# Performance work log

Hardware: AMD Instinct MI355X
Metric: run time of the kernel (lower is better)

Reference implementation:

```python
import jax, jax.numpy as jnp
import numpy as np

B, S, D = 2, 2048, 4096
H, KVH = 32, 8
DH = D // H  # 128
N_REP = H // KVH
ROPE_BASE = 10000.0


def _rope_tables(seq_len, d_head, dtype):
    inv_freq = 1.0 / (ROPE_BASE ** (jnp.arange(0, d_head, 2, dtype=jnp.float32) / d_head))
    pos = jnp.arange(seq_len, dtype=jnp.float32)
    freqs = pos[:, None] * inv_freq[None, :]            # (S, DH/2)
    emb = jnp.concatenate([freqs, freqs], axis=-1)       # (S, DH)
    return jnp.cos(emb).astype(dtype), jnp.sin(emb).astype(dtype)


def _rotate_half(x):
    half = x.shape[-1] // 2
    return jnp.concatenate([-x[..., half:], x[..., :half]], axis=-1)


def _apply_rope(x, cos, sin):
    # x: (B, h, S, DH); cos/sin: (S, DH)
    return x * cos[None, None, :, :] + _rotate_half(x) * sin[None, None, :, :]


def setup_inputs() -> dict:
    key = jax.random.key(0)
    ks = jax.random.split(key, 6)
    scale = 0.02
    return {
        "x": jax.random.normal(ks[0], (B, S, D), dtype=jnp.float32),
        "Wq": jax.random.normal(ks[1], (D, H * DH), dtype=jnp.float32) * scale,
        "Wk": jax.random.normal(ks[2], (D, KVH * DH), dtype=jnp.float32) * scale,
        "Wv": jax.random.normal(ks[3], (D, KVH * DH), dtype=jnp.float32) * scale,
        "Wo": jax.random.normal(ks[4], (D, D), dtype=jnp.float32) * scale,
        "bo": jnp.zeros((D,), dtype=jnp.float32),
    }


def reference(x, Wq, Wk, Wv, Wo, bo):
    b, s, _ = x.shape
    # QKV projections (no bias)
    q = (x @ Wq).reshape(b, s, H, DH).transpose(0, 2, 1, 3)    # (B, H, S, DH)
    k = (x @ Wk).reshape(b, s, KVH, DH).transpose(0, 2, 1, 3)  # (B, KVH, S, DH)
    v = (x @ Wv).reshape(b, s, KVH, DH).transpose(0, 2, 1, 3)
    # RoPE on q and k
    cos, sin = _rope_tables(s, DH, x.dtype)
    q = _apply_rope(q, cos, sin)
    k = _apply_rope(k, cos, sin)
    # GQA: repeat KV heads to match query heads
    k = jnp.repeat(k, N_REP, axis=1)  # (B, H, S, DH)
    v = jnp.repeat(v, N_REP, axis=1)
    # Causal scaled dot-product attention
    scale = 1.0 / jnp.sqrt(jnp.asarray(DH, dtype=x.dtype))
    scores = jnp.einsum("bhqd,bhkd->bhqk", q, k) * scale       # (B, H, S, S)
    causal = jnp.tril(jnp.ones((s, s), dtype=bool))
    scores = jnp.where(causal[None, None, :, :], scores, jnp.finfo(x.dtype).min)
    attn = jax.nn.softmax(scores, axis=-1)
    out = jnp.einsum("bhqk,bhkd->bhqd", attn, v)               # (B, H, S, DH)
    out = out.transpose(0, 2, 1, 3).reshape(b, s, H * DH)
    return out @ Wo + bo
```

## Files before the change

kernel.cpp:

```cpp
#include <hip/hip_runtime.h>

typedef unsigned short u16;
typedef unsigned int u32;
typedef __attribute__((ext_vector_type(8))) short s16x8;
typedef __attribute__((ext_vector_type(8))) u16 u16x8;
typedef __attribute__((ext_vector_type(4))) float f32x4;
typedef __attribute__((ext_vector_type(4))) u32 u32x4;

#define SEQ 2048
#define NH 32
#define NKV 8

__device__ __forceinline__ u16 f2bf(float f) {
  union { float f; u32 u; } v; v.f = f;
  u32 r = v.u + 0x7FFFu + ((v.u >> 16) & 1u);
  return (u16)(r >> 16);
}
__device__ __forceinline__ float bf2f(u16 u) {
  union { u32 u; float f; } v; v.u = ((u32)u) << 16;
  return v.f;
}
__device__ __forceinline__ u32 pack2(float a, float b) {
  return (u32)f2bf(a) | ((u32)f2bf(b) << 16);
}
__device__ __forceinline__ void gll16(u16* lds, const u16* g) {
  __builtin_amdgcn_global_load_lds(
      (const __attribute__((address_space(1))) u32*)g,
      (__attribute__((address_space(3))) u32*)lds, 16, 0, 0);
}

__global__ void k_conv_bf16(const float* __restrict__ in, u16* __restrict__ out) {
  long i = ((long)blockIdx.x * 256 + threadIdx.x) * 4;
  const float4 v = *(const float4*)&in[i];
  ushort4 ov = { f2bf(v.x), f2bf(v.y), f2bf(v.z), f2bf(v.w) };
  *(ushort4*)&out[i] = ov;
}

__global__ void k_transpose_bf16(const float* __restrict__ W, u16* __restrict__ Wt,
                                 int K, int N) {
  __shared__ u16 T[64 * 65];
  int n0 = blockIdx.x * 64, k0 = blockIdx.y * 64;
  int t = threadIdx.x;
  int cr = t >> 4, cc = (t & 15) * 4;
#pragma unroll
  for (int r2 = 0; r2 < 4; ++r2) {
    int k = cr + r2 * 16;
    const float4 v = *(const float4*)&W[(long)(k0 + k) * N + n0 + cc];
    u16* d = &T[k * 65 + cc];
    d[0] = f2bf(v.x); d[1] = f2bf(v.y); d[2] = f2bf(v.z); d[3] = f2bf(v.w);
  }
  __syncthreads();
#pragma unroll
  for (int r2 = 0; r2 < 4; ++r2) {
    int n = cr + r2 * 16;
    ushort4 ov = { T[(cc + 0) * 65 + n], T[(cc + 1) * 65 + n],
                   T[(cc + 2) * 65 + n], T[(cc + 3) * 65 + n] };
    *(ushort4*)&Wt[(long)(n0 + n) * K + k0 + cc] = ov;
  }
}

__global__ void k_vt(const u16* __restrict__ Vb, u16* __restrict__ Vt) {
  __shared__ u16 T[64][136];
  int s0 = blockIdx.x * 64;
  int g = blockIdx.y;
  const u16* src = Vb + (long)g * SEQ * 128;
  u16* dst = Vt + (long)g * 128 * SEQ;
  int t = threadIdx.x;
#pragma unroll
  for (int i = 0; i < 4; ++i) {
    int c = i * 256 + t;
    int row = c >> 4, col8 = (c & 15) * 8;
    u16x8 v = *(const u16x8*)&src[(long)(s0 + row) * 128 + col8];
#pragma unroll
    for (int j = 0; j < 8; ++j) T[row][col8 + j] = v[j];
  }
  __syncthreads();
#pragma unroll
  for (int i = 0; i < 4; ++i) {
    int c = i * 256 + t;
    int d = c >> 3, k8 = (c & 7) * 8;
    u16x8 v;
#pragma unroll
    for (int j = 0; j < 8; ++j) v[j] = T[k8 + j][d];
    *(u16x8*)&dst[(long)d * SEQ + s0 + k8] = v;
  }
}

__global__ void k_rope_table(float* __restrict__ cosT, float* __restrict__ sinT) {
  int id = blockIdx.x * 256 + threadIdx.x;
  int s = id >> 6, i = id & 63;
  float inv = powf(10000.0f, -(float)i * (1.0f / 64.0f));
  float f = (float)s * inv;
  float sv, cv;
  sincosf(f, &sv, &cv);
  cosT[id] = cv; sinT[id] = sv;
}

__global__ void k_rope_apply(u16* __restrict__ Qb, u16* __restrict__ Kb,
                             const float* __restrict__ cosT, const float* __restrict__ sinT) {
  int id = blockIdx.x * 256 + threadIdx.x;
  int i = id & 63;
  int row = id >> 6;
  u16* base = (row < 131072) ? (Qb + (long)row * 128) : (Kb + (long)(row - 131072) * 128);
  int s = row & (SEQ - 1);
  float c = cosT[s * 64 + i], sn = sinT[s * 64 + i];
  float x0 = bf2f(base[i]), x1 = bf2f(base[i + 64]);
  base[i] = f2bf(x0 * c - x1 * sn);
  base[i + 64] = f2bf(x1 * c + x0 * sn);
}

__device__ __forceinline__ void stg(char* smem, int base, const u16* XG, long off,
                                    int K, int tid, int r0, int scol) {
  gll16((u16*)(smem + base + tid * 16), XG + (long)r0 * K + off + scol);
  gll16((u16*)(smem + base + 8192 + tid * 16), XG + (long)(r0 + 128) * K + off + scol);
}

#define GPHASE(MH, KH, READB, STG_STMT, WAIT_STMT)                                  \
  {                                                                                 \
    const char* Ab_ = smem + cbuf + (KH) * 16384;                                   \
    const char* Bb_ = smem + cbuf + 32768 + (KH) * 16384;                           \
    s16x8 Ar_[4];                                                                   \
    _Pragma("unroll")                                                               \
    for (int m_ = 0; m_ < 4; ++m_)                                                  \
      Ar_[m_] = *(const s16x8*)(Ab_ + aoff + ((MH) * 4 + m_) * 1024);               \
    if (READB) {                                                                    \
      _Pragma("unroll")                                                             \
      for (int n_ = 0; n_ < 4; ++n_)                                                \
        Br[n_] = *(const s16x8*)(Bb_ + boff + n_ * 1024);                           \
    }                                                                               \
    STG_STMT;                                                                       \
    __builtin_amdgcn_s_barrier();                                                   \
    asm volatile("s_waitcnt lgkmcnt(0)" ::: "memory");                              \
    __builtin_amdgcn_sched_barrier(0);                                              \
    __builtin_amdgcn_s_setprio(1);                                                  \
    _Pragma("unroll")                                                               \
    for (int m_ = 0; m_ < 4; ++m_) {                                                \
      _Pragma("unroll")                                                             \
      for (int n_ = 0; n_ < 4; ++n_)                                                \
        acc[(MH) * 4 + m_][n_] = __builtin_amdgcn_mfma_f32_16x16x32_bf16(           \
            Ar_[m_], Br[n_], acc[(MH) * 4 + m_][n_], 0, 0, 0);                      \
    }                                                                               \
    __builtin_amdgcn_s_setprio(0);                                                  \
    WAIT_STMT;                                                                      \
    __builtin_amdgcn_s_barrier();                                                   \
  }

template <int MODE>
__global__ __launch_bounds__(512, 1) void k_gemm256(
    const u16* __restrict__ A, const u16* __restrict__ Bt,
    float* __restrict__ Cf, const float* __restrict__ bias,
    u16* __restrict__ Qb, u16* __restrict__ Kb, u16* __restrict__ Vb,
    int K, int nbn) {
  extern __shared__ char smem[];
  int bid = blockIdx.x;
  int cpx = (int)gridDim.x >> 3;
  int swz = (bid & 7) * cpx + (bid >> 3);
  int bm = swz / nbn, bn = swz - bm * nbn;
  int tid = threadIdx.x;
  int lane = tid & 63, wave = tid >> 6;
  int lo = lane & 15, hi = lane >> 4;
  int wm = wave >> 2, wn = wave & 3;
  const u16* Ag = A + (long)bm * 256 * K;
  const u16* Bg = Bt + (long)bn * 256 * K;
  f32x4 zero4 = {0.f, 0.f, 0.f, 0.f};
  f32x4 acc[8][4];
#pragma unroll
  for (int m = 0; m < 8; ++m)
#pragma unroll
    for (int n = 0; n < 4; ++n) acc[m][n] = zero4;

  int aoff = wm * 8192 + ((lo >> 3) << 9) + ((lo & 7) << 4) + (hi << 7);
  int boff = wn * 4096 + ((lo >> 3) << 9) + ((lo & 7) << 4) + (hi << 7);
  int r0 = ((tid >> 5) << 3) + (tid & 7);
  int scol = ((tid >> 3) & 3) << 3;

  int nt = K >> 6;
  stg(smem, 0,             Ag, 0,  K, tid, r0, scol);
  stg(smem, 32768,         Bg, 0,  K, tid, r0, scol);
  stg(smem, 16384,         Ag, 32, K, tid, r0, scol);
  stg(smem, 49152,         Bg, 32, K, tid, r0, scol);
  stg(smem, 65536,         Ag, 64, K, tid, r0, scol);
  stg(smem, 65536 + 32768, Bg, 64, K, tid, r0, scol);
  asm volatile("s_waitcnt vmcnt(4)" ::: "memory");
  __builtin_amdgcn_s_barrier();

  s16x8 Br[4];
  for (int t = 0; t < nt; ++t) {
    int cbuf = (t & 1) << 16;
    int obuf = cbuf ^ 65536;
    long k1 = (long)(t + 1) * 64;
    long k2 = (long)(t + 2) * 64;
    bool s1ok = (t + 1) < nt, s2ok = (t + 2) < nt;
    GPHASE(0, 0, true,
           { if (s1ok) stg(smem, obuf + 16384, Ag, k1 + 32, K, tid, r0, scol); }, {})
    GPHASE(1, 0, false,
           { if (s1ok) stg(smem, obuf + 49152, Bg, k1 + 32, K, tid, r0, scol); }, {})
    GPHASE(0, 1, true,
           { if (s2ok) stg(smem, cbuf, Ag, k2, K, tid, r0, scol); }, {})
    GPHASE(1, 1, false,
           { if (s2ok) stg(smem, cbuf + 32768, Bg, k2, K, tid, r0, scol); },
           {
             if (s2ok)      asm volatile("s_waitcnt vmcnt(4)" ::: "memory");
             else if (s1ok) asm volatile("s_waitcnt vmcnt(0)" ::: "memory");
           })
  }

#pragma unroll
  for (int mr = 0; mr < 8; ++mr) {
#pragma unroll
    for (int n = 0; n < 4; ++n) {
      int colg = bn * 256 + wn * 64 + n * 16 + lo;
#pragma unroll
      for (int r = 0; r < 4; ++r) {
        int rowg = bm * 256 + wm * 128 + mr * 16 + hi * 4 + r;
        float v = acc[mr][n][r];
        if (MODE == 1) {
          Cf[(long)rowg * 4096 + colg] = v + bias[colg];
        } else {
          int bb = rowg >> 11, s = rowg & 2047;
          u16 u = f2bf(v);
          int d = colg & 127;
          if (colg < 4096) {
            int hh = colg >> 7;
            Qb[(((long)bb * NH + hh) * SEQ + s) * 128 + d] = u;
          } else if (colg < 5120) {
            int hh = (colg - 4096) >> 7;
            Kb[(((long)bb * NKV + hh) * SEQ + s) * 128 + d] = u;
          } else {
            int hh = (colg - 5120) >> 7;
            Vb[(((long)bb * NKV + hh) * SEQ + s) * 128 + d] = u;
          }
        }
      }
    }
  }
}

__device__ __forceinline__ void stage_load(u32x4* kr_, u32x4* vr_,
    const u16* __restrict__ Kg, const u16* __restrict__ Vg, int kt, int tid) {
#pragma unroll
  for (int i = 0; i < 4; ++i) {
    int idx = i * 256 + tid;
    int kr = idx >> 4, kc = idx & 15;
    kr_[i] = *(const u32x4*)&Kg[(long)(kt + kr) * 128 + kc * 8];
    int vr = idx >> 3, vc = idx & 7;
    vr_[i] = *(const u32x4*)&Vg[(long)vr * SEQ + kt + vc * 8];
  }
}
__device__ __forceinline__ void stage_write(const u32x4* kr_, const u32x4* vr_,
    u16* Ks, u16* Vs, int tid) {
  char* KsB = (char*)Ks; char* VsB = (char*)Vs;
#pragma unroll
  for (int i = 0; i < 4; ++i) {
    int idx = i * 256 + tid;
    int kr = idx >> 4, kc = idx & 15;
    *(u32x4*)(KsB + ((kr * 256 + kc * 16) ^ ((kr & 7) << 4))) = kr_[i];
    int vr = idx >> 3, vc = idx & 7;
    *(u32x4*)(VsB + ((vr * 128 + vc * 16) ^ ((vr & 7) << 4))) = vr_[i];
  }
}

__global__ __launch_bounds__(256, 2) void k_attn(
    const u16* __restrict__ Qb, const u16* __restrict__ Kb,
    const u16* __restrict__ Vt, u16* __restrict__ AO) {
  __shared__ u16 Ks0[64 * 128], Ks1[64 * 128], Vs0[128 * 64], Vs1[128 * 64];
  __shared__ u16 Ps[4][2][16][32];
  int gid = blockIdx.x;
  int wid = (gid & 7) * 128 + (gid >> 3);
  int g = wid >> 6, w = wid & 63;
  int b = g >> 3, kvh = g & 7;
  int h = kvh * 4 + (w >> 4);
  int qt = 15 - (w & 15);
  int qb0 = qt * 128;
  int tid = threadIdx.x, lane = tid & 63, wave = tid >> 6;
  int lo = lane & 15, hi = lane >> 4;
  int q0w = qb0 + wave * 32;

  const u16* Kg = Kb + (long)(b * NKV + kvh) * SEQ * 128;
  const u16* Vg = Vt + (long)(b * NKV + kvh) * 128 * SEQ;
  const u16* Qg = Qb + (long)(b * NH + h) * SEQ * 128;

  s16x8 qf[2][4];
#pragma unroll
  for (int qs = 0; qs < 2; ++qs)
#pragma unroll
    for (int ds = 0; ds < 4; ++ds)
      qf[qs][ds] = *(const s16x8*)&Qg[(long)(q0w + qs * 16 + lo) * 128 + ds * 32 + hi * 8];

  f32x4 zero4 = {0.f, 0.f, 0.f, 0.f};
  f32x4 o[2][8];
#pragma unroll
  for (int qs = 0; qs < 2; ++qs)
#pragma unroll
    for (int dt = 0; dt < 8; ++dt) o[qs][dt] = zero4;
  float m_run[2] = {-1e30f, -1e30f};
  float l_run[2] = {0.f, 0.f};
  const float scale = 0.088388347648318447f;

  char* PsQ0 = (char*)&Ps[wave][0][0][0];
  char* PsQ1 = (char*)&Ps[wave][1][0][0];
  int pbase = lo << 6;

  u32x4 kreg[4], vreg[4];
  int ntiles = (qb0 >> 6) + 2;
  stage_load(kreg, vreg, Kg, Vg, 0, tid);
  stage_write(kreg, vreg, Ks0, Vs0, tid);
  __syncthreads();

  for (int t = 0; t < ntiles; ++t) {
    int kt = t << 6;
    u16* Ks = (t & 1) ? Ks1 : Ks0;
    u16* Vs = (t & 1) ? Vs1 : Vs0;
    bool more = (t + 1 < ntiles);
    if (more) stage_load(kreg, vreg, Kg, Vg, (t + 1) << 6, tid);
    if (kt <= q0w + 31) {
      f32x4 sa[2][4];
#pragma unroll
      for (int qs = 0; qs < 2; ++qs)
#pragma unroll
        for (int a = 0; a < 4; ++a) sa[qs][a] = zero4;
#pragma unroll
      for (int ds = 0; ds < 4; ++ds) {
        s16x8 kf[4];
#pragma unroll
        for (int a = 0; a < 4; ++a)
          kf[a] = *(const s16x8*)&Ks[((a * 16 + lo) << 7) + (((ds * 4 + hi) ^ (lo & 7)) << 3)];
#pragma unroll
        for (int qs = 0; qs < 2; ++qs)
#pragma unroll
          for (int a = 0; a < 4; ++a)
            sa[qs][a] = __builtin_amdgcn_mfma_f32_16x16x32_bf16(kf[a], qf[qs][ds], sa[qs][a], 0, 0, 0);
      }
      bool pmask = (kt + 63) > q0w;
      u32 pp[2][4][2];
#pragma unroll
      for (int qs = 0; qs < 2; ++qs) {
        float pv[16];
        int qrow = q0w + qs * 16 + lo;
#pragma unroll
        for (int a = 0; a < 4; ++a)
#pragma unroll
          for (int r = 0; r < 4; ++r) {
            float s = sa[qs][a][r] * scale;
            if (pmask && (kt + a * 16 + hi * 4 + r) > qrow) s = -1e30f;
            pv[a * 4 + r] = s;
          }
        float mx = pv[0];
#pragma unroll
        for (int i = 1; i < 16; ++i) mx = fmaxf(mx, pv[i]);
        mx = fmaxf(mx, __shfl_xor(mx, 16));
        mx = fmaxf(mx, __shfl_xor(mx, 32));
        float mnew = fmaxf(m_run[qs], mx);
        if (!__all(mnew - m_run[qs] <= 8.0f)) {
          float corr = __expf(m_run[qs] - mnew);
          m_run[qs] = mnew;
          l_run[qs] *= corr;
#pragma unroll
          for (int dt = 0; dt < 8; ++dt)
#pragma unroll
            for (int r = 0; r < 4; ++r) o[qs][dt][r] *= corr;
        }
        float sum = 0.f;
#pragma unroll
        for (int i = 0; i < 16; ++i) { pv[i] = __expf(pv[i] - m_run[qs]); sum += pv[i]; }
        sum += __shfl_xor(sum, 16);
        sum += __shfl_xor(sum, 32);
        l_run[qs] += sum;
#pragma unroll
        for (int a = 0; a < 4; ++a) {
          pp[qs][a][0] = pack2(pv[a * 4 + 0], pv[a * 4 + 1]);
          pp[qs][a][1] = pack2(pv[a * 4 + 2], pv[a * 4 + 3]);
        }
      }
#pragma unroll
      for (int kb = 0; kb < 2; ++kb) {
#pragma unroll
        for (int qs = 0; qs < 2; ++qs) {
          char* Pw = qs ? PsQ1 : PsQ0;
#pragma unroll
          for (int al = 0; al < 2; ++al) {
            uint2 wv; wv.x = pp[qs][kb * 2 + al][0]; wv.y = pp[qs][kb * 2 + al][1];
            *(uint2*)(Pw + pbase + (((al * 4 + hi) ^ (lo & 7)) << 3)) = wv;
          }
        }
        asm volatile("s_waitcnt lgkmcnt(0)" ::: "memory");
        __builtin_amdgcn_sched_barrier(0);
        union { uint2 u2[2]; s16x8 v; } bu0, bu1;
        bu0.u2[0] = *(uint2*)(PsQ0 + pbase + (((hi * 2 + 0) ^ (lo & 7)) << 3));
        bu0.u2[1] = *(uint2*)(PsQ0 + pbase + (((hi * 2 + 1) ^ (lo & 7)) << 3));
        bu1.u2[0] = *(uint2*)(PsQ1 + pbase + (((hi * 2 + 0) ^ (lo & 7)) << 3));
        bu1.u2[1] = *(uint2*)(PsQ1 + pbase + (((hi * 2 + 1) ^ (lo & 7)) << 3));
#pragma unroll
        for (int dt = 0; dt < 8; ++dt) {
          s16x8 vf = *(const s16x8*)((char*)Vs +
              (((dt * 16 + lo) * 128 + (kb * 4 + hi) * 16) ^ ((lo & 7) << 4)));
          o[0][dt] = __builtin_amdgcn_mfma_f32_16x16x32_bf16(vf, bu0.v, o[0][dt], 0, 0, 0);
          o[1][dt] = __builtin_amdgcn_mfma_f32_16x16x32_bf16(vf, bu1.v, o[1][dt], 0, 0, 0);
        }
      }
    }
    if (more) stage_write(kreg, vreg, (t & 1) ? Ks0 : Ks1, (t & 1) ? Vs0 : Vs1, tid);
    __syncthreads();
  }

#pragma unroll
  for (int qs = 0; qs < 2; ++qs) {
    float inv = 1.0f / l_run[qs];
    long base = ((long)(b * SEQ + q0w + qs * 16 + lo)) * 4096 + h * 128;
#pragma unroll
    for (int dt = 0; dt < 8; ++dt) {
      uint2 wv;
      wv.x = pack2(o[qs][dt][0] * inv, o[qs][dt][1] * inv);
      wv.y = pack2(o[qs][dt][2] * inv, o[qs][dt][3] * inv);
      *(uint2*)&AO[base + dt * 16 + hi * 4] = wv;
    }
  }
}

extern "C" void kernel_launch(void* const* d_in, const int* in_sizes, int n_in,
                              void* d_out, int out_size, void* d_ws, size_t ws_size,
                              hipStream_t stream) {
  const float* x  = (const float*)d_in[0];
  const float* Wq = (const float*)d_in[1];
  const float* Wk = (const float*)d_in[2];
  const float* Wv = (const float*)d_in[3];
  const float* Wo = (const float*)d_in[4];
  const float* bo = (const float*)d_in[5];
  float* out = (float*)d_out;

  char* ws = (char*)d_ws;
  u16* xb     = (u16*)(ws);
  u16* Wt     = (u16*)(ws + 33554432);
  u16* Vtb    = (u16*)(ws + 67108864);
  u16* Qb     = (u16*)(ws + 83886080);
  u16* Kb     = (u16*)(ws + 117440512);
  u16* Vb     = (u16*)(ws + 125829120);
  float* cosT = (float*)(ws + 134217728);
  float* sinT = (float*)(ws + 134742016);
  if (ws_size < 135266304) return;
  u16* AO  = xb;
  u16* Wto = Wt;

  (void)hipFuncSetAttribute((const void*)k_gemm256<0>,
                            hipFuncAttributeMaxDynamicSharedMemorySize, 131072);
  (void)hipFuncSetAttribute((const void*)k_gemm256<1>,
                            hipFuncAttributeMaxDynamicSharedMemorySize, 131072);

  k_conv_bf16<<<16384, 256, 0, stream>>>(x, xb);
  k_transpose_bf16<<<dim3(64, 64), 256, 0, stream>>>(Wq, Wt, 4096, 4096);
  k_transpose_bf16<<<dim3(16, 64), 256, 0, stream>>>(Wk, Wt + (long)4096 * 4096, 4096, 1024);
  k_transpose_bf16<<<dim3(16, 64), 256, 0, stream>>>(Wv, Wt + (long)5120 * 4096, 4096, 1024);
  k_rope_table<<<512, 256, 0, stream>>>(cosT, sinT);
  k_gemm256<0><<<384, 512, 131072, stream>>>(xb, Wt, nullptr, nullptr, Qb, Kb, Vb, 4096, 24);
  k_vt<<<dim3(32, 16), 256, 0, stream>>>(Vb, Vtb);
  k_rope_apply<<<40960, 256, 0, stream>>>(Qb, Kb, cosT, sinT);
  k_transpose_bf16<<<dim3(64, 64), 256, 0, stream>>>(Wo, Wto, 4096, 4096);
  k_attn<<<1024, 256, 0, stream>>>(Qb, Kb, Vtb, AO);
  k_gemm256<1><<<256, 512, 131072, stream>>>(AO, Wto, out, bo, nullptr, nullptr, nullptr, 4096, 16);
}
```

Baseline: 653.5 us.

## Add 128x256 output GEMM kernel and XCD-aware tile mapping for QKV GEMM

Replaces the output-projection GEMM (previously 256x256 tiles, 256 blocks, one block per CU) with a new 128x256-tile kernel that uses a simple double-buffered K=32 pipeline and 48KB LDS. It launches 512 blocks with two blocks per CU, so more CUs are busy and waves overlap. The QKV GEMM gets a hardcoded XCD-grouped block-to-tile mapping and pointer-increment addressing to cut address arithmetic. The new kernel waits with vmcnt(0) every iteration, which exposes load latency more than the deeper pipeline it replaces did.

```diff
diff --git a/kernel.cpp b/kernel.cpp
--- a/kernel.cpp
+++ b/kernel.cpp
@@ -10,6 +10,8 @@
 #define SEQ 2048
 #define NH 32
 #define NKV 8
+#define AS1 __attribute__((address_space(1)))
+#define AS3 __attribute__((address_space(3)))
 
 __device__ __forceinline__ u16 f2bf(float f) {
   union { float f; u32 u; } v; v.f = f;
@@ -22,11 +24,6 @@
 }
 __device__ __forceinline__ u32 pack2(float a, float b) {
   return (u32)f2bf(a) | ((u32)f2bf(b) << 16);
-}
-__device__ __forceinline__ void gll16(u16* lds, const u16* g) {
-  __builtin_amdgcn_global_load_lds(
-      (const __attribute__((address_space(1))) u32*)g,
-      (__attribute__((address_space(3))) u32*)lds, 16, 0, 0);
 }
 
 __global__ void k_conv_bf16(const float* __restrict__ in, u16* __restrict__ out) {
@@ -109,11 +106,11 @@
   base[i + 64] = f2bf(x1 * c + x0 * sn);
 }
 
-__device__ __forceinline__ void stg(char* smem, int base, const u16* XG, long off,
-                                    int K, int tid, int r0, int scol) {
-  gll16((u16*)(smem + base + tid * 16), XG + (long)r0 * K + off + scol);
-  gll16((u16*)(smem + base + 8192 + tid * 16), XG + (long)(r0 + 128) * K + off + scol);
-}
+#define STG2(base_, pl_, ph_, D_)                                                    \
+  { __builtin_amdgcn_global_load_lds((const AS1 u32*)((pl_) + (D_)),                 \
+        (AS3 u32*)(smem + (base_) + tid * 16), 16, 0, 0);                            \
+    __builtin_amdgcn_global_load_lds((const AS1 u32*)((ph_) + (D_)),                 \
+        (AS3 u32*)(smem + (base_) + 8192 + tid * 16), 16, 0, 0); }
 
 #define GPHASE(MH, KH, READB, STG_STMT, WAIT_STMT)                                  \
   {                                                                                 \
@@ -145,17 +142,14 @@
     __builtin_amdgcn_s_barrier();                                                   \
   }
 
-template <int MODE>
 __global__ __launch_bounds__(512, 1) void k_gemm256(
     const u16* __restrict__ A, const u16* __restrict__ Bt,
-    float* __restrict__ Cf, const float* __restrict__ bias,
-    u16* __restrict__ Qb, u16* __restrict__ Kb, u16* __restrict__ Vb,
-    int K, int nbn) {
+    u16* __restrict__ Qb, u16* __restrict__ Kb, u16* __restrict__ Vb, int K) {
   extern __shared__ char smem[];
   int bid = blockIdx.x;
-  int cpx = (int)gridDim.x >> 3;
-  int swz = (bid & 7) * cpx + (bid >> 3);
-  int bm = swz / nbn, bn = swz - bm * nbn;
+  int xc = bid & 7, c = bid >> 3;
+  int bm = (xc >> 1) * 4 + c / 12;
+  int bn = (xc & 1) * 12 + c % 12;
   int tid = threadIdx.x;
   int lane = tid & 63, wave = tid >> 6;
   int lo = lane & 15, hi = lane >> 4;
@@ -173,14 +167,18 @@
   int boff = wn * 4096 + ((lo >> 3) << 9) + ((lo & 7) << 4) + (hi << 7);
   int r0 = ((tid >> 5) << 3) + (tid & 7);
   int scol = ((tid >> 3) & 3) << 3;
+  const u16* aL = Ag + (long)r0 * K + scol;
+  const u16* aH = aL + (long)128 * K;
+  const u16* bL = Bg + (long)r0 * K + scol;
+  const u16* bH = bL + (long)128 * K;
 
   int nt = K >> 6;
-  stg(smem, 0,             Ag, 0,  K, tid, r0, scol);
-  stg(smem, 32768,         Bg, 0,  K, tid, r0, scol);
-  stg(smem, 16384,         Ag, 32, K, tid, r0, scol);
-  stg(smem, 49152,         Bg, 32, K, tid, r0, scol);
-  stg(smem, 65536,         Ag, 64, K, tid, r0, scol);
-  stg(smem, 65536 + 32768, Bg, 64, K, tid, r0, scol);
+  STG2(0,             aL, aH, 0);
+  STG2(32768,         bL, bH, 0);
+  STG2(16384,         aL, aH, 32);
+  STG2(49152,         bL, bH, 32);
+  STG2(65536,         aL, aH, 64);
+  STG2(65536 + 32768, bL, bH, 64);
   asm volatile("s_waitcnt vmcnt(4)" ::: "memory");
   __builtin_amdgcn_s_barrier();
 
@@ -188,21 +186,20 @@
   for (int t = 0; t < nt; ++t) {
     int cbuf = (t & 1) << 16;
     int obuf = cbuf ^ 65536;
-    long k1 = (long)(t + 1) * 64;
-    long k2 = (long)(t + 2) * 64;
     bool s1ok = (t + 1) < nt, s2ok = (t + 2) < nt;
     GPHASE(0, 0, true,
-           { if (s1ok) stg(smem, obuf + 16384, Ag, k1 + 32, K, tid, r0, scol); }, {})
+           { if (s1ok) STG2(obuf + 16384, aL, aH, 96); }, {})
     GPHASE(1, 0, false,
-           { if (s1ok) stg(smem, obuf + 49152, Bg, k1 + 32, K, tid, r0, scol); }, {})
+           { if (s1ok) STG2(obuf + 49152, bL, bH, 96); }, {})
     GPHASE(0, 1, true,
-           { if (s2ok) stg(smem, cbuf, Ag, k2, K, tid, r0, scol); }, {})
+           { if (s2ok) STG2(cbuf, aL, aH, 128); }, {})
     GPHASE(1, 1, false,
-           { if (s2ok) stg(smem, cbuf + 32768, Bg, k2, K, tid, r0, scol); },
+           { if (s2ok) STG2(cbuf + 32768, bL, bH, 128); },
            {
              if (s2ok)      asm volatile("s_waitcnt vmcnt(4)" ::: "memory");
              else if (s1ok) asm volatile("s_waitcnt vmcnt(0)" ::: "memory");
            })
+    aL += 64; aH += 64; bL += 64; bH += 64;
   }
 
 #pragma unroll
@@ -214,26 +211,103 @@
       for (int r = 0; r < 4; ++r) {
         int rowg = bm * 256 + wm * 128 + mr * 16 + hi * 4 + r;
         float v = acc[mr][n][r];
-        if (MODE == 1) {
-          Cf[(long)rowg * 4096 + colg] = v + bias[colg];
+        int bb = rowg >> 11, s = rowg & 2047;
+        u16 u = f2bf(v);
+        int d = colg & 127;
+        if (colg < 4096) {
+          int hh = colg >> 7;
+          Qb[(((long)bb * NH + hh) * SEQ + s) * 128 + d] = u;
+        } else if (colg < 5120) {
+          int hh = (colg - 4096) >> 7;
+          Kb[(((long)bb * NKV + hh) * SEQ + s) * 128 + d] = u;
         } else {
-          int bb = rowg >> 11, s = rowg & 2047;
-          u16 u = f2bf(v);
-          int d = colg & 127;
-          if (colg < 4096) {
-            int hh = colg >> 7;
-            Qb[(((long)bb * NH + hh) * SEQ + s) * 128 + d] = u;
-          } else if (colg < 5120) {
-            int hh = (colg - 4096) >> 7;
-            Kb[(((long)bb * NKV + hh) * SEQ + s) * 128 + d] = u;
-          } else {
-            int hh = (colg - 5120) >> 7;
-            Vb[(((long)bb * NKV + hh) * SEQ + s) * 128 + d] = u;
-          }
+          int hh = (colg - 5120) >> 7;
+          Vb[(((long)bb * NKV + hh) * SEQ + s) * 128 + d] = u;
         }
       }
     }
   }
+}
+
+__global__ __launch_bounds__(512, 2) void k_gemm128(
+    const u16* __restrict__ A, const u16* __restrict__ Bt,
+    float* __restrict__ Cf, const float* __restrict__ bias, int K) {
+  extern __shared__ char smem[];
+  int bid = blockIdx.x;
+  int xc = bid & 7, c = bid >> 3;
+  int bm = (xc >> 1) * 8 + (c >> 3);
+  int bn = (xc & 1) * 8 + (c & 7);
+  int tid = threadIdx.x;
+  int lane = tid & 63, wave = tid >> 6;
+  int lo = lane & 15, hi = lane >> 4;
+  int wm = wave >> 2, wn = wave & 3;
+  const u16* Ag = A + (long)bm * 128 * K;
+  const u16* Bg = Bt + (long)bn * 256 * K;
+  f32x4 zero4 = {0.f, 0.f, 0.f, 0.f};
+  f32x4 acc[4][4];
+#pragma unroll
+  for (int m = 0; m < 4; ++m)
+#pragma unroll
+    for (int n = 0; n < 4; ++n) acc[m][n] = zero4;
+
+  int aoff = wm * 4096 + ((lo >> 3) << 9) + ((lo & 7) << 4) + (hi << 7);
+  int boff = 8192 + wn * 4096 + ((lo >> 3) << 9) + ((lo & 7) << 4) + (hi << 7);
+  int r0 = ((tid >> 5) << 3) + (tid & 7);
+  int scol = ((tid >> 3) & 3) << 3;
+  const u16* aP  = Ag + (long)r0 * K + scol;
+  const u16* bP0 = Bg + (long)r0 * K + scol;
+  const u16* bP1 = bP0 + (long)128 * K;
+
+#define G128STG(nxt_, D_)                                                            \
+  { __builtin_amdgcn_global_load_lds((const AS1 u32*)(aP + (D_)),                    \
+        (AS3 u32*)(smem + (nxt_) + tid * 16), 16, 0, 0);                             \
+    __builtin_amdgcn_global_load_lds((const AS1 u32*)(bP0 + (D_)),                   \
+        (AS3 u32*)(smem + (nxt_) + 8192 + tid * 16), 16, 0, 0);                      \
+    __builtin_amdgcn_global_load_lds((const AS1 u32*)(bP1 + (D_)),                   \
+        (AS3 u32*)(smem + (nxt_) + 16384 + tid * 16), 16, 0, 0); }
+
+  int nt = K >> 5;
+  G128STG(0, 0);
+  asm volatile("s_waitcnt vmcnt(0)" ::: "memory");
+  __builtin_amdgcn_s_barrier();
+
+  for (int t = 0; t < nt; ++t) {
+    int cur = (t & 1) * 24576;
+    int nxt = cur ^ 24576;
+    bool more = (t + 1) < nt;
+    if (more) G128STG(nxt, 32);
+    s16x8 Af[4], Bf[4];
+#pragma unroll
+    for (int m = 0; m < 4; ++m) Af[m] = *(const s16x8*)(smem + cur + aoff + m * 1024);
+#pragma unroll
+    for (int n = 0; n < 4; ++n) Bf[n] = *(const s16x8*)(smem + cur + boff + n * 1024);
+    asm volatile("s_waitcnt lgkmcnt(0)" ::: "memory");
+    __builtin_amdgcn_sched_barrier(0);
+    __builtin_amdgcn_s_setprio(1);
+#pragma unroll
+    for (int m = 0; m < 4; ++m)
+#pragma unroll
+      for (int n = 0; n < 4; ++n)
+        acc[m][n] = __builtin_amdgcn_mfma_f32_16x16x32_bf16(Af[m], Bf[n], acc[m][n], 0, 0, 0);
+    __builtin_amdgcn_s_setprio(0);
+    if (more) asm volatile("s_waitcnt vmcnt(0)" ::: "memory");
+    __builtin_amdgcn_s_barrier();
+    aP += 32; bP0 += 32; bP1 += 32;
+  }
+
+#pragma unroll
+  for (int m = 0; m < 4; ++m) {
+#pragma unroll
+    for (int n = 0; n < 4; ++n) {
+      int colg = bn * 256 + wn * 64 + n * 16 + lo;
+#pragma unroll
+      for (int r = 0; r < 4; ++r) {
+        int rowg = bm * 128 + wm * 64 + m * 16 + hi * 4 + r;
+        Cf[(long)rowg * 4096 + colg] = acc[m][n][r] + bias[colg];
+      }
+    }
+  }
+#undef G128STG
 }
 
 __device__ __forceinline__ void stage_load(u32x4* kr_, u32x4* vr_,
@@ -441,9 +515,7 @@
   u16* AO  = xb;
   u16* Wto = Wt;
 
-  (void)hipFuncSetAttribute((const void*)k_gemm256<0>,
-                            hipFuncAttributeMaxDynamicSharedMemorySize, 131072);
-  (void)hipFuncSetAttribute((const void*)k_gemm256<1>,
+  (void)hipFuncSetAttribute((const void*)k_gemm256,
                             hipFuncAttributeMaxDynamicSharedMemorySize, 131072);
 
   k_conv_bf16<<<16384, 256, 0, stream>>>(x, xb);
@@ -451,10 +523,10 @@
   k_transpose_bf16<<<dim3(16, 64), 256, 0, stream>>>(Wk, Wt + (long)4096 * 4096, 4096, 1024);
   k_transpose_bf16<<<dim3(16, 64), 256, 0, stream>>>(Wv, Wt + (long)5120 * 4096, 4096, 1024);
   k_rope_table<<<512, 256, 0, stream>>>(cosT, sinT);
-  k_gemm256<0><<<384, 512, 131072, stream>>>(xb, Wt, nullptr, nullptr, Qb, Kb, Vb, 4096, 24);
+  k_gemm256<<<384, 512, 131072, stream>>>(xb, Wt, Qb, Kb, Vb, 4096);
   k_vt<<<dim3(32, 16), 256, 0, stream>>>(Vb, Vtb);
   k_rope_apply<<<40960, 256, 0, stream>>>(Qb, Kb, cosT, sinT);
   k_transpose_bf16<<<dim3(64, 64), 256, 0, stream>>>(Wo, Wto, 4096, 4096);
   k_attn<<<1024, 256, 0, stream>>>(Qb, Kb, Vtb, AO);
-  k_gemm256<1><<<256, 512, 131072, stream>>>(AO, Wto, out, bo, nullptr, nullptr, nullptr, 4096, 16);
-}
+  k_gemm128<<<512, 512, 49152, stream>>>(AO, Wto, out, bo, 4096);
+}
```

Result: slower. 700.6 us (+7.2%).

## Remap GEMM tiles per XCD, precompute load pointers, issue loads after MFMAs

Applied to the files above, without the earlier changes.

Replaces the block swizzle so each XCD gets a compact rectangle of output tiles (4 row-blocks by half the column-blocks), improving L2 reuse of A and B tiles within an XCD. Load addresses are precomputed as per-thread pointers advanced each k-iteration, removing 64-bit address math from the loop. Global-to-LDS stage issue is moved after the MFMA block within each phase, changing overlap between loads and compute, which may delay prefetch issue.

```diff
diff --git a/kernel.cpp b/kernel.cpp
--- a/kernel.cpp
+++ b/kernel.cpp
@@ -10,6 +10,8 @@
 #define SEQ 2048
 #define NH 32
 #define NKV 8
+#define AS1 __attribute__((address_space(1)))
+#define AS3 __attribute__((address_space(3)))
 
 __device__ __forceinline__ u16 f2bf(float f) {
   union { float f; u32 u; } v; v.f = f;
@@ -22,11 +24,6 @@
 }
 __device__ __forceinline__ u32 pack2(float a, float b) {
   return (u32)f2bf(a) | ((u32)f2bf(b) << 16);
-}
-__device__ __forceinline__ void gll16(u16* lds, const u16* g) {
-  __builtin_amdgcn_global_load_lds(
-      (const __attribute__((address_space(1))) u32*)g,
-      (__attribute__((address_space(3))) u32*)lds, 16, 0, 0);
 }
 
 __global__ void k_conv_bf16(const float* __restrict__ in, u16* __restrict__ out) {
@@ -109,11 +106,11 @@
   base[i + 64] = f2bf(x1 * c + x0 * sn);
 }
 
-__device__ __forceinline__ void stg(char* smem, int base, const u16* XG, long off,
-                                    int K, int tid, int r0, int scol) {
-  gll16((u16*)(smem + base + tid * 16), XG + (long)r0 * K + off + scol);
-  gll16((u16*)(smem + base + 8192 + tid * 16), XG + (long)(r0 + 128) * K + off + scol);
-}
+#define STG2(base_, pl_, ph_, D_)                                                    \
+  { __builtin_amdgcn_global_load_lds((const AS1 u32*)((pl_) + (D_)),                 \
+        (AS3 u32*)(smem + (base_) + tid * 16), 16, 0, 0);                            \
+    __builtin_amdgcn_global_load_lds((const AS1 u32*)((ph_) + (D_)),                 \
+        (AS3 u32*)(smem + (base_) + 8192 + tid * 16), 16, 0, 0); }
 
 #define GPHASE(MH, KH, READB, STG_STMT, WAIT_STMT)                                  \
   {                                                                                 \
@@ -128,7 +125,6 @@
       for (int n_ = 0; n_ < 4; ++n_)                                                \
         Br[n_] = *(const s16x8*)(Bb_ + boff + n_ * 1024);                           \
     }                                                                               \
-    STG_STMT;                                                                       \
     __builtin_amdgcn_s_barrier();                                                   \
     asm volatile("s_waitcnt lgkmcnt(0)" ::: "memory");                              \
     __builtin_amdgcn_sched_barrier(0);                                              \
@@ -141,6 +137,7 @@
             Ar_[m_], Br[n_], acc[(MH) * 4 + m_][n_], 0, 0, 0);                      \
     }                                                                               \
     __builtin_amdgcn_s_setprio(0);                                                  \
+    STG_STMT;                                                                       \
     WAIT_STMT;                                                                      \
     __builtin_amdgcn_s_barrier();                                                   \
   }
@@ -150,12 +147,12 @@
     const u16* __restrict__ A, const u16* __restrict__ Bt,
     float* __restrict__ Cf, const float* __restrict__ bias,
     u16* __restrict__ Qb, u16* __restrict__ Kb, u16* __restrict__ Vb,
-    int K, int nbn) {
+    int K, int bnP) {
   extern __shared__ char smem[];
   int bid = blockIdx.x;
-  int cpx = (int)gridDim.x >> 3;
-  int swz = (bid & 7) * cpx + (bid >> 3);
-  int bm = swz / nbn, bn = swz - bm * nbn;
+  int xc = bid & 7, c = bid >> 3;
+  int bm = (xc >> 1) * 4 + c / bnP;
+  int bn = (xc & 1) * bnP + c % bnP;
   int tid = threadIdx.x;
   int lane = tid & 63, wave = tid >> 6;
   int lo = lane & 15, hi = lane >> 4;
@@ -173,14 +170,18 @@
   int boff = wn * 4096 + ((lo >> 3) << 9) + ((lo & 7) << 4) + (hi << 7);
   int r0 = ((tid >> 5) << 3) + (tid & 7);
   int scol = ((tid >> 3) & 3) << 3;
+  const u16* aL = Ag + (long)r0 * K + scol;
+  const u16* aH = aL + (long)128 * K;
+  const u16* bL = Bg + (long)r0 * K + scol;
+  const u16* bH = bL + (long)128 * K;
 
   int nt = K >> 6;
-  stg(smem, 0,             Ag, 0,  K, tid, r0, scol);
-  stg(smem, 32768,         Bg, 0,  K, tid, r0, scol);
-  stg(smem, 16384,         Ag, 32, K, tid, r0, scol);
-  stg(smem, 49152,         Bg, 32, K, tid, r0, scol);
-  stg(smem, 65536,         Ag, 64, K, tid, r0, scol);
-  stg(smem, 65536 + 32768, Bg, 64, K, tid, r0, scol);
+  STG2(0,             aL, aH, 0);
+  STG2(32768,         bL, bH, 0);
+  STG2(16384,         aL, aH, 32);
+  STG2(49152,         bL, bH, 32);
+  STG2(65536,         aL, aH, 64);
+  STG2(65536 + 32768, bL, bH, 64);
   asm volatile("s_waitcnt vmcnt(4)" ::: "memory");
   __builtin_amdgcn_s_barrier();
 
@@ -188,21 +189,20 @@
   for (int t = 0; t < nt; ++t) {
     int cbuf = (t & 1) << 16;
     int obuf = cbuf ^ 65536;
-    long k1 = (long)(t + 1) * 64;
-    long k2 = (long)(t + 2) * 64;
     bool s1ok = (t + 1) < nt, s2ok = (t + 2) < nt;
     GPHASE(0, 0, true,
-           { if (s1ok) stg(smem, obuf + 16384, Ag, k1 + 32, K, tid, r0, scol); }, {})
+           { if (s1ok) STG2(obuf + 16384, aL, aH, 96); }, {})
     GPHASE(1, 0, false,
-           { if (s1ok) stg(smem, obuf + 49152, Bg, k1 + 32, K, tid, r0, scol); }, {})
+           { if (s1ok) STG2(obuf + 49152, bL, bH, 96); }, {})
     GPHASE(0, 1, true,
-           { if (s2ok) stg(smem, cbuf, Ag, k2, K, tid, r0, scol); }, {})
+           { if (s2ok) STG2(cbuf, aL, aH, 128); }, {})
     GPHASE(1, 1, false,
-           { if (s2ok) stg(smem, cbuf + 32768, Bg, k2, K, tid, r0, scol); },
+           { if (s2ok) STG2(cbuf + 32768, bL, bH, 128); },
            {
              if (s2ok)      asm volatile("s_waitcnt vmcnt(4)" ::: "memory");
              else if (s1ok) asm volatile("s_waitcnt vmcnt(0)" ::: "memory");
            })
+    aL += 64; aH += 64; bL += 64; bH += 64;
   }
 
 #pragma unroll
@@ -451,10 +451,10 @@
   k_transpose_bf16<<<dim3(16, 64), 256, 0, stream>>>(Wk, Wt + (long)4096 * 4096, 4096, 1024);
   k_transpose_bf16<<<dim3(16, 64), 256, 0, stream>>>(Wv, Wt + (long)5120 * 4096, 4096, 1024);
   k_rope_table<<<512, 256, 0, stream>>>(cosT, sinT);
-  k_gemm256<0><<<384, 512, 131072, stream>>>(xb, Wt, nullptr, nullptr, Qb, Kb, Vb, 4096, 24);
+  k_gemm256<0><<<384, 512, 131072, stream>>>(xb, Wt, nullptr, nullptr, Qb, Kb, Vb, 4096, 12);
   k_vt<<<dim3(32, 16), 256, 0, stream>>>(Vb, Vtb);
   k_rope_apply<<<40960, 256, 0, stream>>>(Qb, Kb, cosT, sinT);
   k_transpose_bf16<<<dim3(64, 64), 256, 0, stream>>>(Wo, Wto, 4096, 4096);
   k_attn<<<1024, 256, 0, stream>>>(Qb, Kb, Vtb, AO);
-  k_gemm256<1><<<256, 512, 131072, stream>>>(AO, Wto, out, bo, nullptr, nullptr, nullptr, 4096, 16);
-}
+  k_gemm256<1><<<256, 512, 131072, stream>>>(AO, Wto, out, bo, nullptr, nullptr, nullptr, 4096, 8);
+}
```

New measurement: 654.4 us. Within noise of the previous version (+0.1%).
